# Kernel optimization log

Measured on AMD Instinct MI355X. Metric: run time of the kernel, lower is better.

## Reference

```python
import jax, jax.numpy as jnp
import numpy as np

NEG = -1e30
H = 768

def mask_logits(target, mask):
    return target * mask + (1.0 - mask) * NEG

def setup_inputs() -> dict:
    key = jax.random.key(0)
    ks = jax.random.split(key, 8)
    B, CL, QL = 16, 512, 64
    c = jax.random.normal(ks[0], (B, CL, H), dtype=jnp.float32)
    q = jax.random.normal(ks[1], (B, QL, H), dtype=jnp.float32)
    c_mask = jnp.ones((B, CL), dtype=jnp.float32)
    q_mask = jnp.ones((B, QL), dtype=jnp.float32)
    # nn.Linear(768,1) weights (kaiming-ish scale) and biases
    std = 1.0 / np.sqrt(H)
    w_c = jax.random.normal(ks[2], (H,), dtype=jnp.float32) * std
    w_q = jax.random.normal(ks[3], (H,), dtype=jnp.float32) * std
    w_cq = jax.random.normal(ks[4], (H,), dtype=jnp.float32) * std
    b_c = jax.random.normal(ks[5], (), dtype=jnp.float32) * std
    b_q = jax.random.normal(ks[6], (), dtype=jnp.float32) * std
    b_cq = jax.random.normal(ks[7], (), dtype=jnp.float32) * std
    return {"c": c, "q": q, "c_mask": c_mask, "q_mask": q_mask,
            "w_c": w_c, "b_c": b_c, "w_q": w_q, "b_q": b_q,
            "w_cq": w_cq, "b_cq": b_cq}

def reference(c, q, c_mask, q_mask, w_c, b_c, w_q, b_q, w_cq, b_cq):
    # c: (B, c_len, H), q: (B, q_len, H)
    cm = c_mask[:, :, None]   # (B, c_len, 1)
    qm = q_mask[:, None, :]   # (B, 1, q_len)
    # per-query loop in torch == trilinear term: ((c*w_cq) @ q^T) + b_cq
    cq = jnp.einsum('bid,bjd->bij', c * w_cq, q) + b_cq      # (B, c_len, q_len)
    s = (c @ w_c + b_c)[:, :, None] + (q @ w_q + b_q)[:, None, :] + cq
    a = jax.nn.softmax(mask_logits(s, qm), axis=2)            # (B, c_len, q_len)
    c2q = jnp.einsum('bij,bjd->bid', a, q)                    # (B, c_len, H)
    b_att = jax.nn.softmax(jnp.max(mask_logits(s, cm), axis=2), axis=1)  # (B, c_len)
    q2c = jnp.einsum('bi,bid->bd', b_att, c)[:, None, :]      # (B, 1, H)
    x = jnp.concatenate([c, c2q, c * c2q, c * q2c], axis=-1)  # (B, c_len, 4H)
    return x
```

## Files before the change

### kernel.cpp

```cpp
#include <hip/hip_runtime.h>
#include <math.h>
#include <stdint.h>

#define NEGV -1e30f
typedef unsigned short u16;
typedef unsigned int u32;
typedef short bfx8 __attribute__((ext_vector_type(8)));
typedef float f32x4 __attribute__((ext_vector_type(4)));

constexpr int B_  = 16;
constexpr int CL  = 512;
constexpr int QL  = 64;
constexpr int H   = 768;
constexpr int OD  = 4 * H;
constexpr int IT  = 16;
constexpr int OSTR = 772;

constexpr size_t WS_QW     = 0;
constexpr size_t WS_ROWMAX = 1024;
constexpr size_t WS_BATT   = 9216;
constexpr size_t WS_PART   = 17408;
constexpr size_t WS_Q2C    = 410624;
constexpr size_t WS_QB     = 422912;
constexpr size_t WS_QT     = 816128;

__device__ __forceinline__ u16 f2b(float x) {
  u32 u = __float_as_uint(x);
  u += 0x7FFFu + ((u >> 16) & 1u);
  return (u16)(u >> 16);
}
__device__ __forceinline__ float wredmax(float v) {
#pragma unroll
  for (int off = 32; off; off >>= 1) v = fmaxf(v, __shfl_xor(v, off));
  return v;
}
__device__ __forceinline__ float wredsum(float v) {
#pragma unroll
  for (int off = 32; off; off >>= 1) v += __shfl_xor(v, off);
  return v;
}

__global__ __launch_bounds__(256) void k_qw(const float* __restrict__ q,
                                            const float* __restrict__ w_q,
                                            const float* __restrict__ b_q,
                                            const float* __restrict__ b_cq,
                                            float* __restrict__ qw) {
  int w = threadIdx.x >> 6, lane = threadIdx.x & 63;
  int row = blockIdx.x * 4 + w;
  const float* qr = q + (size_t)row * H;
  float s = 0.f;
  for (int d = lane; d < H; d += 64) s += qr[d] * w_q[d];
#pragma unroll
  for (int off = 32; off; off >>= 1) s += __shfl_xor(s, off);
  if (lane == 0) qw[row] = s + b_q[0] + b_cq[0];
}

__global__ __launch_bounds__(256) void k_qprep(const float* __restrict__ q,
                                               const float* __restrict__ w_cq,
                                               u16* __restrict__ qb,
                                               u16* __restrict__ qT) {
  __shared__ u16 tile[64 * 132];
  const int ch = blockIdx.x, bb = blockIdx.y, t = threadIdx.x;
  const int d0 = ch * 128;
#pragma unroll
  for (int s = 0; s < 8; ++s) {
    int idx = t + s * 256;
    int j = idx >> 5, d4 = idx & 31;
    size_t go = ((size_t)(bb * QL + j)) * H + d0 + d4 * 4;
    float4 v = *(const float4*)(q + go);
    float4 w = *(const float4*)(w_cq + d0 + d4 * 4);
    uint2 raw, scl;
    raw.x = f2b(v.x) | ((u32)f2b(v.y) << 16);
    raw.y = f2b(v.z) | ((u32)f2b(v.w) << 16);
    scl.x = f2b(v.x * w.x) | ((u32)f2b(v.y * w.y) << 16);
    scl.y = f2b(v.z * w.z) | ((u32)f2b(v.w * w.w) << 16);
    *(uint2*)(qb + go) = scl;
    *(uint2*)&tile[j * 132 + d4 * 4] = raw;
  }
  __syncthreads();
  const int dr = t >> 1, half = t & 1;
#pragma unroll
  for (int g = 0; g < 4; ++g) {
    u16 tmp[8];
#pragma unroll
    for (int e = 0; e < 8; ++e) tmp[e] = tile[(half * 32 + g * 8 + e) * 132 + dr];
    uint4 o;
    o.x = tmp[0] | ((u32)tmp[1] << 16); o.y = tmp[2] | ((u32)tmp[3] << 16);
    o.z = tmp[4] | ((u32)tmp[5] << 16); o.w = tmp[6] | ((u32)tmp[7] << 16);
    *(uint4*)(qT + ((size_t)bb * H + d0 + dr) * QL + half * 32 + g * 8) = o;
  }
}

__global__ __launch_bounds__(256, 2) void ka(const float* __restrict__ c,
                                             const float* __restrict__ c_mask,
                                             const float* __restrict__ q_mask,
                                             const float* __restrict__ w_c,
                                             const float* __restrict__ b_c,
                                             const float* __restrict__ qw,
                                             const u16* __restrict__ qb,
                                             const u16* __restrict__ qT,
                                             float* __restrict__ rowmax,
                                             float* __restrict__ out) {
  __shared__ __align__(16) char shm[IT * OSTR * 4];
  __shared__ float sS[IT * 68];
  __shared__ u16 aS[IT * 64];
  u16* cA = (u16*)shm;
  float* oS = (float*)shm;

  const int t = threadIdx.x, lane = t & 63;
  const int wid = __builtin_amdgcn_readfirstlane(t >> 6);
  const int bb = blockIdx.y, i0 = blockIdx.x * IT;
  const int lr = lane & 15, lg = lane >> 4;
  const int sw = (lr & 7) << 4;

  {
    int row = t >> 4, c4b = t & 15;
    size_t cb0 = ((size_t)bb * CL + i0 + row) * H;
#pragma unroll
    for (int u = 0; u < 12; ++u) {
      int col4 = c4b + u * 16;
      float4 v = *(const float4*)(c + cb0 + col4 * 4);
      uint2 pk;
      pk.x = f2b(v.x) | ((u32)f2b(v.y) << 16);
      pk.y = f2b(v.z) | ((u32)f2b(v.w) << 16);
      int byte = row * 1536 + ((col4 * 8) ^ ((row & 7) << 4));
      *(uint2*)((char*)cA + byte) = pk;
    }
  }
  const float qw_r = qw[bb * QL + lane];
  const float qm_r = q_mask[bb * QL + lane];
  __syncthreads();

  f32x4 acc0 = {0.f, 0.f, 0.f, 0.f}, acc1 = {0.f, 0.f, 0.f, 0.f};
  {
    const u16* qbp = qb + ((size_t)bb * QL + wid * 16 + lr) * H + lg * 8;
    const char* ap = (const char*)cA + lr * 1536;
#pragma unroll
    for (int k0 = 0; k0 < 768; k0 += 64) {
      bfx8 av0 = *(const bfx8*)(ap + ((k0 * 2 + lg * 16) ^ sw));
      bfx8 bv0 = *(const bfx8*)(qbp + k0);
      bfx8 av1 = *(const bfx8*)(ap + (((k0 + 32) * 2 + lg * 16) ^ sw));
      bfx8 bv1 = *(const bfx8*)(qbp + k0 + 32);
      acc0 = __builtin_amdgcn_mfma_f32_16x16x32_bf16(av0, bv0, acc0, 0, 0, 0);
      acc1 = __builtin_amdgcn_mfma_f32_16x16x32_bf16(av1, bv1, acc1, 0, 0, 0);
    }
  }
#pragma unroll
  for (int m = 0; m < 4; ++m)
    sS[(lg * 4 + m) * 68 + wid * 16 + lr] = acc0[m] + acc1[m];

  float cwv[4];
#pragma unroll
  for (int rr = 0; rr < 4; ++rr) {
    size_t ro = ((size_t)bb * CL + i0 + wid * 4 + rr) * H;
    float p = 0.f;
#pragma unroll
    for (int pi = 0; pi < 3; ++pi) {
      int k = pi * 256 + lane * 4;
      float4 cv = *(const float4*)(c + ro + k);
      float4 wv = *(const float4*)(w_c + k);
      p += cv.x * wv.x + cv.y * wv.y + cv.z * wv.z + cv.w * wv.w;
    }
    cwv[rr] = wredsum(p);
  }
  const float bc = b_c[0];
  __syncthreads();

#pragma unroll
  for (int rr = 0; rr < 4; ++rr) {
    int r = wid * 4 + rr;
    float s = sS[r * 68 + lane] + qw_r;
    float mraw = wredmax(s);
    float sm = (qm_r > 0.5f) ? s : NEGV;
    float mm = wredmax(sm);
    float p = __expf(sm - mm);
    float ps = wredsum(p);
    float a = p / ps;
    if (lane == 0) {
      float cmv = c_mask[bb * CL + i0 + r];
      rowmax[bb * CL + i0 + r] = (cmv > 0.5f) ? (mraw + cwv[rr] + bc) : NEGV;
    }
    int byte = r * 128 + ((lane * 2) ^ ((r & 7) << 4));
    *(u16*)((char*)aS + byte) = f2b(a);
  }
  __syncthreads();

  bfx8 a0 = *(const bfx8*)((char*)aS + lr * 128 + ((lg * 16) ^ sw));
  bfx8 a1 = *(const bfx8*)((char*)aS + lr * 128 + ((64 + lg * 16) ^ sw));
  const u16* qTp = qT + (size_t)bb * H * QL;
  f32x4 o[12];
#pragma unroll
  for (int u = 0; u < 12; ++u) {
    int dR = (wid * 12 + u) * 16 + lr;
    bfx8 b0 = *(const bfx8*)(qTp + (size_t)dR * QL + lg * 8);
    bfx8 b1 = *(const bfx8*)(qTp + (size_t)dR * QL + 32 + lg * 8);
    f32x4 v = {0.f, 0.f, 0.f, 0.f};
    v = __builtin_amdgcn_mfma_f32_16x16x32_bf16(a0, b0, v, 0, 0, 0);
    v = __builtin_amdgcn_mfma_f32_16x16x32_bf16(a1, b1, v, 0, 0, 0);
    o[u] = v;
  }
  __syncthreads();

#pragma unroll
  for (int u = 0; u < 12; ++u) {
    int d = wid * 192 + u * 16 + lr;
#pragma unroll
    for (int m = 0; m < 4; ++m)
      oS[(lg * 4 + m) * OSTR + d] = o[u][m];
  }
  __syncthreads();
  {
    int row = t >> 4, c4b = t & 15;
    size_t grow = (size_t)bb * CL + i0 + row;
    const float* crow = c + grow * H;
    float* ob = out + grow * OD;
#pragma unroll
    for (int k = 0; k < 12; ++k) {
      int d = (c4b + k * 16) * 4;
      float4 cv = *(const float4*)(crow + d);
      float4 ov = *(const float4*)&oS[row * OSTR + d];
      *(float4*)(ob + d) = cv;
      *(float4*)(ob + H + d) = ov;
      *(float4*)(ob + 2 * H + d) = make_float4(cv.x * ov.x, cv.y * ov.y,
                                               cv.z * ov.z, cv.w * ov.w);
    }
  }
}

__global__ __launch_bounds__(256) void kb1(const float* __restrict__ rowmax,
                                           float* __restrict__ batt) {
  int b = blockIdx.x, t = threadIdx.x;
  __shared__ float red[4];
  float v0 = rowmax[b * CL + t], v1 = rowmax[b * CL + t + 256];
  float m = fmaxf(v0, v1);
#pragma unroll
  for (int off = 32; off; off >>= 1) m = fmaxf(m, __shfl_xor(m, off));
  if ((t & 63) == 0) red[t >> 6] = m;
  __syncthreads();
  m = fmaxf(fmaxf(red[0], red[1]), fmaxf(red[2], red[3]));
  float p0 = __expf(v0 - m), p1 = __expf(v1 - m);
  float s = p0 + p1;
#pragma unroll
  for (int off = 32; off; off >>= 1) s += __shfl_xor(s, off);
  __syncthreads();
  if ((t & 63) == 0) red[t >> 6] = s;
  __syncthreads();
  s = red[0] + red[1] + red[2] + red[3];
  float inv = 1.0f / s;
  batt[b * CL + t] = p0 * inv;
  batt[b * CL + t + 256] = p1 * inv;
}

__global__ __launch_bounds__(192) void kb2(const float* __restrict__ c,
                                           const float* __restrict__ batt,
                                           float* __restrict__ part) {
  int s = blockIdx.x, b = blockIdx.y, t = threadIdx.x;
  __shared__ float ba[16];
  if (t < 16) ba[t] = batt[b * CL + s * 16 + t];
  __syncthreads();
  const float* cb = c + ((size_t)b * CL + s * 16) * H;
  float4 acc = make_float4(0.f, 0.f, 0.f, 0.f);
#pragma unroll
  for (int r = 0; r < 16; ++r) {
    float w = ba[r];
    float4 cv = *(const float4*)(cb + (size_t)r * H + t * 4);
    acc.x += w * cv.x; acc.y += w * cv.y; acc.z += w * cv.z; acc.w += w * cv.w;
  }
  *(float4*)(part + ((size_t)b * 32 + s) * H + t * 4) = acc;
}

__global__ __launch_bounds__(256) void kb3(const float* __restrict__ part,
                                           float* __restrict__ q2c) {
  int b = blockIdx.x / 3, third = blockIdx.x % 3, t = threadIdx.x;
  int d = third * 256 + t;
  float s = 0.f;
  for (int k = 0; k < 32; ++k) s += part[((size_t)b * 32 + k) * H + d];
  q2c[b * H + d] = s;
}

__global__ __launch_bounds__(256) void kc(const float* __restrict__ c,
                                          const float* __restrict__ q2c,
                                          float* __restrict__ out) {
  const float4* c4 = (const float4*)c;
  const float4* g4 = (const float4*)q2c;
  float4* o4 = (float4*)out;
  int idx = blockIdx.x * 256 + threadIdx.x;
#pragma unroll
  for (int k = 0; k < 3; ++k, idx += 2048 * 256) {
    int row = idx / 192, dq = idx - row * 192;
    int b = row >> 9;
    float4 cv = c4[(size_t)row * 192 + dq];
    float4 gv = g4[b * 192 + dq];
    float4 r;
    r.x = cv.x * gv.x; r.y = cv.y * gv.y; r.z = cv.z * gv.z; r.w = cv.w * gv.w;
    o4[(size_t)row * 768 + 576 + dq] = r;
  }
}

extern "C" void kernel_launch(void* const* d_in, const int* in_sizes, int n_in,
                              void* d_out, int out_size, void* d_ws, size_t ws_size,
                              hipStream_t stream) {
  const float* c      = (const float*)d_in[0];
  const float* q      = (const float*)d_in[1];
  const float* c_mask = (const float*)d_in[2];
  const float* q_mask = (const float*)d_in[3];
  const float* w_c    = (const float*)d_in[4];
  const float* b_c    = (const float*)d_in[5];
  const float* w_q    = (const float*)d_in[6];
  const float* b_q    = (const float*)d_in[7];
  const float* w_cq   = (const float*)d_in[8];
  const float* b_cq   = (const float*)d_in[9];
  float* out = (float*)d_out;
  float* ws  = (float*)d_ws;
  float* qw     = ws + WS_QW;
  float* rowmax = ws + WS_ROWMAX;
  float* batt   = ws + WS_BATT;
  float* part   = ws + WS_PART;
  float* q2c    = ws + WS_Q2C;
  u16*   qb     = (u16*)(ws + WS_QB);
  u16*   qT     = (u16*)(ws + WS_QT);

  k_qw<<<256, 256, 0, stream>>>(q, w_q, b_q, b_cq, qw);
  k_qprep<<<dim3(6, B_), 256, 0, stream>>>(q, w_cq, qb, qT);
  ka<<<dim3(CL / IT, B_), 256, 0, stream>>>(c, c_mask, q_mask, w_c, b_c,
                                            qw, qb, qT, rowmax, out);
  kb1<<<B_, 256, 0, stream>>>(rowmax, batt);
  kb2<<<dim3(32, B_), 192, 0, stream>>>(c, batt, part);
  kb3<<<B_ * 3, 256, 0, stream>>>(part, q2c);
  kc<<<2048, 256, 0, stream>>>(c, q2c, out);
}
```

Measured before the change: 64.63 us.

## Pre-swizzle Q operands into MFMA fragment order and fuse small kernels

The q preparation kernel now writes the scaled and transposed bf16 copies of q directly in MFMA fragment order, so the attention kernel loads each B operand as one contiguous 16-byte read per lane. The q·w_q projection becomes an extra block of the prep kernel, and the c·w_c dot product is folded into the c staging loop instead of re-reading c from global memory. The column-softmax kernel is merged into the weighted-sum kernel, which recomputes the max and sum in every block. The output staging buffer is halved by writing it out in two passes, which lowers LDS use and may allow more resident blocks, at the cost of an extra barrier and redundant softmax work per block.

Result: faster. 61.13 us (-5.4%).

```diff
diff --git a/kernel.cpp b/kernel.cpp
--- a/kernel.cpp
+++ b/kernel.cpp
@@ -18,11 +18,10 @@
 
 constexpr size_t WS_QW     = 0;
 constexpr size_t WS_ROWMAX = 1024;
-constexpr size_t WS_BATT   = 9216;
 constexpr size_t WS_PART   = 17408;
 constexpr size_t WS_Q2C    = 410624;
-constexpr size_t WS_QB     = 422912;
-constexpr size_t WS_QT     = 816128;
+constexpr size_t WS_QBF    = 422912;
+constexpr size_t WS_QTF    = 816128;
 
 __device__ __forceinline__ u16 f2b(float x) {
   u32 u = __float_as_uint(x);
@@ -40,32 +39,35 @@
   return v;
 }
 
-__global__ __launch_bounds__(256) void k_qw(const float* __restrict__ q,
-                                            const float* __restrict__ w_q,
-                                            const float* __restrict__ b_q,
-                                            const float* __restrict__ b_cq,
-                                            float* __restrict__ qw) {
-  int w = threadIdx.x >> 6, lane = threadIdx.x & 63;
-  int row = blockIdx.x * 4 + w;
-  const float* qr = q + (size_t)row * H;
-  float s = 0.f;
-  for (int d = lane; d < H; d += 64) s += qr[d] * w_q[d];
-#pragma unroll
-  for (int off = 32; off; off >>= 1) s += __shfl_xor(s, off);
-  if (lane == 0) qw[row] = s + b_q[0] + b_cq[0];
-}
-
 __global__ __launch_bounds__(256) void k_qprep(const float* __restrict__ q,
                                                const float* __restrict__ w_cq,
-                                               u16* __restrict__ qb,
-                                               u16* __restrict__ qT) {
-  __shared__ u16 tile[64 * 132];
+                                               const float* __restrict__ w_q,
+                                               const float* __restrict__ b_q,
+                                               const float* __restrict__ b_cq,
+                                               u16* __restrict__ qbF,
+                                               u16* __restrict__ qTF,
+                                               float* __restrict__ qw) {
   const int ch = blockIdx.x, bb = blockIdx.y, t = threadIdx.x;
+  if (ch == 6) {
+    int j = t >> 2, qt = t & 3;
+    const float* qr = q + ((size_t)bb * QL + j) * H;
+    float s = 0.f;
+#pragma unroll 8
+    for (int p = 0; p < 48; ++p) {
+      float4 v = *(const float4*)(qr + (qt * 48 + p) * 4);
+      float4 w = *(const float4*)(w_q + (qt * 48 + p) * 4);
+      s += v.x * w.x + v.y * w.y + v.z * w.z + v.w * w.w;
+    }
+    s += __shfl_xor(s, 1);
+    s += __shfl_xor(s, 2);
+    if (qt == 0) qw[bb * QL + j] = s + b_q[0] + b_cq[0];
+    return;
+  }
+  __shared__ u16 tR[64 * 132], tS[64 * 132];
   const int d0 = ch * 128;
 #pragma unroll
-  for (int s = 0; s < 8; ++s) {
-    int idx = t + s * 256;
-    int j = idx >> 5, d4 = idx & 31;
+  for (int s2 = 0; s2 < 8; ++s2) {
+    int idx = t + s2 * 256, j = idx >> 5, d4 = idx & 31;
     size_t go = ((size_t)(bb * QL + j)) * H + d0 + d4 * 4;
     float4 v = *(const float4*)(q + go);
     float4 w = *(const float4*)(w_cq + d0 + d4 * 4);
@@ -74,20 +76,43 @@
     raw.y = f2b(v.z) | ((u32)f2b(v.w) << 16);
     scl.x = f2b(v.x * w.x) | ((u32)f2b(v.y * w.y) << 16);
     scl.y = f2b(v.z * w.z) | ((u32)f2b(v.w * w.w) << 16);
-    *(uint2*)(qb + go) = scl;
-    *(uint2*)&tile[j * 132 + d4 * 4] = raw;
-  }
-  __syncthreads();
-  const int dr = t >> 1, half = t & 1;
-#pragma unroll
-  for (int g = 0; g < 4; ++g) {
-    u16 tmp[8];
-#pragma unroll
-    for (int e = 0; e < 8; ++e) tmp[e] = tile[(half * 32 + g * 8 + e) * 132 + dr];
-    uint4 o;
-    o.x = tmp[0] | ((u32)tmp[1] << 16); o.y = tmp[2] | ((u32)tmp[3] << 16);
-    o.z = tmp[4] | ((u32)tmp[5] << 16); o.w = tmp[6] | ((u32)tmp[7] << 16);
-    *(uint4*)(qT + ((size_t)bb * H + d0 + dr) * QL + half * 32 + g * 8) = o;
+    *(uint2*)&tR[j * 132 + d4 * 4] = raw;
+    *(uint2*)&tS[j * 132 + d4 * 4] = scl;
+  }
+  __syncthreads();
+  {
+    int l = t & 63, jt = t >> 6, lr = l & 15, lg = l >> 4;
+#pragma unroll
+    for (int kt = 0; kt < 4; ++kt) {
+      u16 vals[8];
+#pragma unroll
+      for (int e = 0; e < 8; ++e)
+        vals[e] = tS[(jt * 16 + lr) * 132 + kt * 32 + lg * 8 + e];
+      uint4 pk;
+      pk.x = vals[0] | ((u32)vals[1] << 16);
+      pk.y = vals[2] | ((u32)vals[3] << 16);
+      pk.z = vals[4] | ((u32)vals[5] << 16);
+      pk.w = vals[6] | ((u32)vals[7] << 16);
+      *(uint4*)(qbF + ((((size_t)bb * 4 + jt) * 24) + ch * 4 + kt) * 512 + l * 8) = pk;
+    }
+  }
+  {
+#pragma unroll
+    for (int rep = 0; rep < 4; ++rep) {
+      int idx = rep * 256 + t;
+      int l = idx & 63, h = (idx >> 6) & 1, uul = idx >> 7;
+      int lr = l & 15, lg = l >> 4;
+      u16 vals[8];
+#pragma unroll
+      for (int e = 0; e < 8; ++e)
+        vals[e] = tR[(h * 32 + lg * 8 + e) * 132 + uul * 16 + lr];
+      uint4 pk;
+      pk.x = vals[0] | ((u32)vals[1] << 16);
+      pk.y = vals[2] | ((u32)vals[3] << 16);
+      pk.z = vals[4] | ((u32)vals[5] << 16);
+      pk.w = vals[6] | ((u32)vals[7] << 16);
+      *(uint4*)(qTF + (((size_t)bb * 48 + ch * 8 + uul) * 2 + h) * 512 + l * 8) = pk;
+    }
   }
 }
 
@@ -97,14 +122,13 @@
                                              const float* __restrict__ w_c,
                                              const float* __restrict__ b_c,
                                              const float* __restrict__ qw,
-                                             const u16* __restrict__ qb,
-                                             const u16* __restrict__ qT,
+                                             const u16* __restrict__ qbF,
+                                             const u16* __restrict__ qTF,
                                              float* __restrict__ rowmax,
                                              float* __restrict__ out) {
-  __shared__ __align__(16) char shm[IT * OSTR * 4];
+  __shared__ __align__(16) char shm[8 * OSTR * 4];
   __shared__ float sS[IT * 68];
   __shared__ u16 aS[IT * 64];
-  u16* cA = (u16*)shm;
   float* oS = (float*)shm;
 
   const int t = threadIdx.x, lane = t & 63;
@@ -113,6 +137,7 @@
   const int lr = lane & 15, lg = lane >> 4;
   const int sw = (lr & 7) << 4;
 
+  float cwq = 0.f;
   {
     int row = t >> 4, c4b = t & 15;
     size_t cb0 = ((size_t)bb * CL + i0 + row) * H;
@@ -120,27 +145,34 @@
     for (int u = 0; u < 12; ++u) {
       int col4 = c4b + u * 16;
       float4 v = *(const float4*)(c + cb0 + col4 * 4);
+      float4 w = *(const float4*)(w_c + col4 * 4);
+      cwq += v.x * w.x + v.y * w.y + v.z * w.z + v.w * w.w;
       uint2 pk;
       pk.x = f2b(v.x) | ((u32)f2b(v.y) << 16);
       pk.y = f2b(v.z) | ((u32)f2b(v.w) << 16);
       int byte = row * 1536 + ((col4 * 8) ^ ((row & 7) << 4));
-      *(uint2*)((char*)cA + byte) = pk;
-    }
+      *(uint2*)(shm + byte) = pk;
+    }
+    cwq += __shfl_xor(cwq, 1);
+    cwq += __shfl_xor(cwq, 2);
+    cwq += __shfl_xor(cwq, 4);
+    cwq += __shfl_xor(cwq, 8);
   }
   const float qw_r = qw[bb * QL + lane];
   const float qm_r = q_mask[bb * QL + lane];
+  const float bc = b_c[0];
   __syncthreads();
 
   f32x4 acc0 = {0.f, 0.f, 0.f, 0.f}, acc1 = {0.f, 0.f, 0.f, 0.f};
   {
-    const u16* qbp = qb + ((size_t)bb * QL + wid * 16 + lr) * H + lg * 8;
-    const char* ap = (const char*)cA + lr * 1536;
-#pragma unroll
-    for (int k0 = 0; k0 < 768; k0 += 64) {
-      bfx8 av0 = *(const bfx8*)(ap + ((k0 * 2 + lg * 16) ^ sw));
-      bfx8 bv0 = *(const bfx8*)(qbp + k0);
-      bfx8 av1 = *(const bfx8*)(ap + (((k0 + 32) * 2 + lg * 16) ^ sw));
-      bfx8 bv1 = *(const bfx8*)(qbp + k0 + 32);
+    const u16* qbp = qbF + (((size_t)bb * 4 + wid) * 24) * 512 + lane * 8;
+    const char* ap = shm + lr * 1536;
+#pragma unroll
+    for (int kt = 0; kt < 24; kt += 2) {
+      bfx8 av0 = *(const bfx8*)(ap + ((kt * 64 + lg * 16) ^ sw));
+      bfx8 av1 = *(const bfx8*)(ap + (((kt + 1) * 64 + lg * 16) ^ sw));
+      bfx8 bv0 = *(const bfx8*)(qbp + kt * 512);
+      bfx8 bv1 = *(const bfx8*)(qbp + (kt + 1) * 512);
       acc0 = __builtin_amdgcn_mfma_f32_16x16x32_bf16(av0, bv0, acc0, 0, 0, 0);
       acc1 = __builtin_amdgcn_mfma_f32_16x16x32_bf16(av1, bv1, acc1, 0, 0, 0);
     }
@@ -148,22 +180,6 @@
 #pragma unroll
   for (int m = 0; m < 4; ++m)
     sS[(lg * 4 + m) * 68 + wid * 16 + lr] = acc0[m] + acc1[m];
-
-  float cwv[4];
-#pragma unroll
-  for (int rr = 0; rr < 4; ++rr) {
-    size_t ro = ((size_t)bb * CL + i0 + wid * 4 + rr) * H;
-    float p = 0.f;
-#pragma unroll
-    for (int pi = 0; pi < 3; ++pi) {
-      int k = pi * 256 + lane * 4;
-      float4 cv = *(const float4*)(c + ro + k);
-      float4 wv = *(const float4*)(w_c + k);
-      p += cv.x * wv.x + cv.y * wv.y + cv.z * wv.z + cv.w * wv.w;
-    }
-    cwv[rr] = wredsum(p);
-  }
-  const float bc = b_c[0];
   __syncthreads();
 
 #pragma unroll
@@ -176,9 +192,10 @@
     float p = __expf(sm - mm);
     float ps = wredsum(p);
     float a = p / ps;
+    float cwr = __shfl(cwq, rr * 16);
     if (lane == 0) {
       float cmv = c_mask[bb * CL + i0 + r];
-      rowmax[bb * CL + i0 + r] = (cmv > 0.5f) ? (mraw + cwv[rr] + bc) : NEGV;
+      rowmax[bb * CL + i0 + r] = (cmv > 0.5f) ? (mraw + cwr + bc) : NEGV;
     }
     int byte = r * 128 + ((lane * 2) ^ ((r & 7) << 4));
     *(u16*)((char*)aS + byte) = f2b(a);
@@ -187,38 +204,40 @@
 
   bfx8 a0 = *(const bfx8*)((char*)aS + lr * 128 + ((lg * 16) ^ sw));
   bfx8 a1 = *(const bfx8*)((char*)aS + lr * 128 + ((64 + lg * 16) ^ sw));
-  const u16* qTp = qT + (size_t)bb * H * QL;
+  const u16* qtp = qTF + (size_t)bb * 49152 + lane * 8;
   f32x4 o[12];
 #pragma unroll
   for (int u = 0; u < 12; ++u) {
-    int dR = (wid * 12 + u) * 16 + lr;
-    bfx8 b0 = *(const bfx8*)(qTp + (size_t)dR * QL + lg * 8);
-    bfx8 b1 = *(const bfx8*)(qTp + (size_t)dR * QL + 32 + lg * 8);
+    int uu = wid * 12 + u;
+    bfx8 b0 = *(const bfx8*)(qtp + (size_t)uu * 1024);
+    bfx8 b1 = *(const bfx8*)(qtp + (size_t)uu * 1024 + 512);
     f32x4 v = {0.f, 0.f, 0.f, 0.f};
     v = __builtin_amdgcn_mfma_f32_16x16x32_bf16(a0, b0, v, 0, 0, 0);
     v = __builtin_amdgcn_mfma_f32_16x16x32_bf16(a1, b1, v, 0, 0, 0);
     o[u] = v;
   }
-  __syncthreads();
-
-#pragma unroll
-  for (int u = 0; u < 12; ++u) {
-    int d = wid * 192 + u * 16 + lr;
-#pragma unroll
-    for (int m = 0; m < 4; ++m)
-      oS[(lg * 4 + m) * OSTR + d] = o[u][m];
-  }
-  __syncthreads();
-  {
-    int row = t >> 4, c4b = t & 15;
-    size_t grow = (size_t)bb * CL + i0 + row;
+
+#pragma unroll
+  for (int p = 0; p < 2; ++p) {
+    if (p) __syncthreads();
+#pragma unroll
+    for (int u = 0; u < 12; ++u) {
+      int d = wid * 192 + u * 16 + lr;
+      oS[(lg * 2 + 0) * OSTR + d] = o[u][2 * p];
+      oS[(lg * 2 + 1) * OSTR + d] = o[u][2 * p + 1];
+    }
+    __syncthreads();
+    int row8 = t >> 5, c32 = t & 31;
+    int g = row8 >> 1, mo = row8 & 1;
+    int ri = g * 4 + 2 * p + mo;
+    size_t grow = (size_t)bb * CL + i0 + ri;
     const float* crow = c + grow * H;
     float* ob = out + grow * OD;
 #pragma unroll
-    for (int k = 0; k < 12; ++k) {
-      int d = (c4b + k * 16) * 4;
+    for (int k = 0; k < 6; ++k) {
+      int d = (c32 + k * 32) * 4;
       float4 cv = *(const float4*)(crow + d);
-      float4 ov = *(const float4*)&oS[row * OSTR + d];
+      float4 ov = *(const float4*)&oS[row8 * OSTR + d];
       *(float4*)(ob + d) = cv;
       *(float4*)(ob + H + d) = ov;
       *(float4*)(ob + 2 * H + d) = make_float4(cv.x * ov.x, cv.y * ov.y,
@@ -227,46 +246,35 @@
   }
 }
 
-__global__ __launch_bounds__(256) void kb1(const float* __restrict__ rowmax,
-                                           float* __restrict__ batt) {
-  int b = blockIdx.x, t = threadIdx.x;
-  __shared__ float red[4];
+__global__ __launch_bounds__(256) void kb(const float* __restrict__ rowmax,
+                                          const float* __restrict__ c,
+                                          float* __restrict__ part) {
+  int s = blockIdx.x, b = blockIdx.y, t = threadIdx.x;
+  __shared__ float red[8];
+  __shared__ float ba[16];
   float v0 = rowmax[b * CL + t], v1 = rowmax[b * CL + t + 256];
-  float m = fmaxf(v0, v1);
-#pragma unroll
-  for (int off = 32; off; off >>= 1) m = fmaxf(m, __shfl_xor(m, off));
+  float m = wredmax(fmaxf(v0, v1));
   if ((t & 63) == 0) red[t >> 6] = m;
   __syncthreads();
   m = fmaxf(fmaxf(red[0], red[1]), fmaxf(red[2], red[3]));
-  float p0 = __expf(v0 - m), p1 = __expf(v1 - m);
-  float s = p0 + p1;
-#pragma unroll
-  for (int off = 32; off; off >>= 1) s += __shfl_xor(s, off);
-  __syncthreads();
-  if ((t & 63) == 0) red[t >> 6] = s;
-  __syncthreads();
-  s = red[0] + red[1] + red[2] + red[3];
-  float inv = 1.0f / s;
-  batt[b * CL + t] = p0 * inv;
-  batt[b * CL + t + 256] = p1 * inv;
-}
-
-__global__ __launch_bounds__(192) void kb2(const float* __restrict__ c,
-                                           const float* __restrict__ batt,
-                                           float* __restrict__ part) {
-  int s = blockIdx.x, b = blockIdx.y, t = threadIdx.x;
-  __shared__ float ba[16];
-  if (t < 16) ba[t] = batt[b * CL + s * 16 + t];
-  __syncthreads();
-  const float* cb = c + ((size_t)b * CL + s * 16) * H;
-  float4 acc = make_float4(0.f, 0.f, 0.f, 0.f);
-#pragma unroll
-  for (int r = 0; r < 16; ++r) {
-    float w = ba[r];
-    float4 cv = *(const float4*)(cb + (size_t)r * H + t * 4);
-    acc.x += w * cv.x; acc.y += w * cv.y; acc.z += w * cv.z; acc.w += w * cv.w;
-  }
-  *(float4*)(part + ((size_t)b * 32 + s) * H + t * 4) = acc;
+  float p = __expf(v0 - m) + __expf(v1 - m);
+  p = wredsum(p);
+  if ((t & 63) == 0) red[4 + (t >> 6)] = p;
+  __syncthreads();
+  float ssum = red[4] + red[5] + red[6] + red[7];
+  if (t < 16) ba[t] = __expf(rowmax[b * CL + s * 16 + t] - m) / ssum;
+  __syncthreads();
+  if (t < 192) {
+    const float* cb = c + ((size_t)b * CL + s * 16) * H;
+    float4 acc = make_float4(0.f, 0.f, 0.f, 0.f);
+#pragma unroll
+    for (int r = 0; r < 16; ++r) {
+      float w = ba[r];
+      float4 cv = *(const float4*)(cb + (size_t)r * H + t * 4);
+      acc.x += w * cv.x; acc.y += w * cv.y; acc.z += w * cv.z; acc.w += w * cv.w;
+    }
+    *(float4*)(part + ((size_t)b * 32 + s) * H + t * 4) = acc;
+  }
 }
 
 __global__ __launch_bounds__(256) void kb3(const float* __restrict__ part,
@@ -314,18 +322,15 @@
   float* ws  = (float*)d_ws;
   float* qw     = ws + WS_QW;
   float* rowmax = ws + WS_ROWMAX;
-  float* batt   = ws + WS_BATT;
   float* part   = ws + WS_PART;
   float* q2c    = ws + WS_Q2C;
-  u16*   qb     = (u16*)(ws + WS_QB);
-  u16*   qT     = (u16*)(ws + WS_QT);
-
-  k_qw<<<256, 256, 0, stream>>>(q, w_q, b_q, b_cq, qw);
-  k_qprep<<<dim3(6, B_), 256, 0, stream>>>(q, w_cq, qb, qT);
+  u16*   qbF    = (u16*)(ws + WS_QBF);
+  u16*   qTF    = (u16*)(ws + WS_QTF);
+
+  k_qprep<<<dim3(7, B_), 256, 0, stream>>>(q, w_cq, w_q, b_q, b_cq, qbF, qTF, qw);
   ka<<<dim3(CL / IT, B_), 256, 0, stream>>>(c, c_mask, q_mask, w_c, b_c,
-                                            qw, qb, qT, rowmax, out);
-  kb1<<<B_, 256, 0, stream>>>(rowmax, batt);
-  kb2<<<dim3(32, B_), 192, 0, stream>>>(c, batt, part);
+                                            qw, qbF, qTF, rowmax, out);
+  kb<<<dim3(32, B_), 256, 0, stream>>>(rowmax, c, part);
   kb3<<<B_ * 3, 256, 0, stream>>>(part, q2c);
   kc<<<2048, 256, 0, stream>>>(c, q2c, out);
 }
```
